# Kernel optimization log

Hardware: AMD Instinct MI355X
Metric: run time of the kernel (lower is better)

## Reference

```python
import jax, jax.numpy as jnp
import numpy as np

P = 2  # sampling ratio: keep top ceil(M/p) measurements


def setup_inputs() -> dict:
    key = jax.random.key(0)
    k1, k2, k3 = jax.random.split(key, 3)
    B, H, W, C = 8, 1024, 1024, 3
    Y = jax.random.normal(k1, (B, H, W, C), dtype=jnp.float32)
    # build()-time Z0 components: abs ~ N(0.5, 0.1), angle ~ N(0, 0.5*sqrt(pi))
    Z0_abs = 0.5 + 0.1 * jax.random.normal(k2, (1, 1, H, W), dtype=jnp.float32)
    Z0_angle = (0.5 * np.pi ** 0.5) * jax.random.normal(k3, (1, 1, H, W), dtype=jnp.float32)
    return {"Y": Y, "Z0_abs": Z0_abs, "Z0_angle": Z0_angle}


def _make_Z0(Z0_abs, Z0_angle):
    # Z0 = |Z0| * exp(i*angle), Frobenius-normalized over spatial axes (2,3)
    Z0 = Z0_abs.astype(jnp.complex64) * jnp.exp(1j * Z0_angle.astype(jnp.complex64))
    fro = jnp.sqrt(jnp.sum(jnp.abs(Z0) ** 2, axis=(2, 3), keepdims=True)).astype(jnp.complex64)
    return Z0 / fro


def reference(Y, Z0_abs, Z0_angle):
    B, H, W, C = Y.shape
    M = H * W * C
    R = int(np.ceil(M / P))
    # transpose NHWC -> NCHW, scale by original S[2] (= W)
    Y_S = jnp.transpose(Y.astype(jnp.float32), (0, 3, 1, 2)) / jnp.float32(W)
    y_s = Y_S.reshape(B, M)
    # threshold = R-th largest value per batch (== descending-sorted index R-1)
    thr = jax.lax.top_k(y_s, R)[0][:, -1]  # [B]
    Ytr = (Y_S >= thr[:, None, None, None]).astype(jnp.float32)  # [B,C,H,W]
    Z0 = _make_Z0(Z0_abs, Z0_angle)
    return Ytr, Z0
```

## Files before the change

kernel.cpp:

```cpp
#include <hip/hip_runtime.h>
#include <math.h>

#define BATCH 8
#define HH 1024
#define WW 1024
#define CC 3
#define MTOT (HH*WW*CC)
#define RSEL 1572864u

#define WCAP 131072u
#define LCAP 1024u
#define P1B  1024
#define QPT  8

#define U_HI 0xBC800000u
#define U_LO 0x437FFFFFu

typedef float nfloat4 __attribute__((ext_vector_type(4)));
typedef float nfloat2 __attribute__((ext_vector_type(2)));

#define WS_WCNT_OFF  0u
#define WS_CHI_OFF   512u
#define WS_NPART_OFF 1024u
#define WS_THR_OFF   2048u
#define WS_FB_OFF    2112u
#define WS_NORM_OFF  2176u
#define WS_WU_OFF    4096u
#define WS_WP_OFF    4198400u

#define NCOPY 3
#define HSTRIDE 4097

__device__ __forceinline__ unsigned int fmap(float x) {
    unsigned int b = __float_as_uint(x);
    return (b & 0x80000000u) ? ~b : (b | 0x80000000u);
}

__device__ __forceinline__ void nt_store4(float4 v, float4* p) {
    nfloat4 t; t.x = v.x; t.y = v.y; t.z = v.z; t.w = v.w;
    __builtin_nontemporal_store(t, (nfloat4*)p);
}
__device__ __forceinline__ void nt_store2(float2 v, float2* p) {
    nfloat2 t; t.x = v.x; t.y = v.y;
    __builtin_nontemporal_store(t, (nfloat2*)p);
}

__device__ __forceinline__ void thresh_row_quad(const float* __restrict__ Yb,
                                                float* __restrict__ outb,
                                                int h, int w4, unsigned int tu) {
    const float4* src = (const float4*)(Yb + ((size_t)h * WW + (size_t)w4 * 4) * CC);
    float4 a0 = src[0], a1 = src[1], a2 = src[2];
    float4 r0, r1, r2;
    r0.x = (fmap(a0.x) >= tu) ? 1.f : 0.f;
    r0.y = (fmap(a0.w) >= tu) ? 1.f : 0.f;
    r0.z = (fmap(a1.z) >= tu) ? 1.f : 0.f;
    r0.w = (fmap(a2.y) >= tu) ? 1.f : 0.f;
    r1.x = (fmap(a0.y) >= tu) ? 1.f : 0.f;
    r1.y = (fmap(a1.x) >= tu) ? 1.f : 0.f;
    r1.z = (fmap(a1.w) >= tu) ? 1.f : 0.f;
    r1.w = (fmap(a2.z) >= tu) ? 1.f : 0.f;
    r2.x = (fmap(a0.z) >= tu) ? 1.f : 0.f;
    r2.y = (fmap(a1.y) >= tu) ? 1.f : 0.f;
    r2.z = (fmap(a2.x) >= tu) ? 1.f : 0.f;
    r2.w = (fmap(a2.w) >= tu) ? 1.f : 0.f;
    size_t base = (size_t)h * WW;
    ((float4*)(outb + base))[w4]                        = r0;
    ((float4*)(outb + base + (size_t)HH * WW))[w4]      = r1;
    ((float4*)(outb + base + (size_t)2 * HH * WW))[w4]  = r2;
}

__global__ void pass1_kernel(const float* __restrict__ Y,
                             const float* __restrict__ zabs,
                             float* __restrict__ out,
                             unsigned int* __restrict__ wu,
                             unsigned int* __restrict__ wpos,
                             unsigned int* __restrict__ wcnt,
                             unsigned int* __restrict__ chib,
                             float* __restrict__ npart) {
    const int tid = threadIdx.x;

    if (blockIdx.x >= P1B) {
        const int bx = blockIdx.x - P1B;
        float s = 0.f;
        const int n4z = HH * WW / 4;
        for (int i = bx * 256 + tid; i < n4z; i += 256 * 256) {
            float4 v = ((const float4*)zabs)[i];
            s += v.x * v.x + v.y * v.y + v.z * v.z + v.w * v.w;
        }
        for (int d = 32; d > 0; d >>= 1) s += __shfl_down(s, d);
        __shared__ float ls[4];
        if ((tid & 63) == 0) ls[tid >> 6] = s;
        __syncthreads();
        if (tid == 0) npart[bx] = ls[0] + ls[1] + ls[2] + ls[3];
        return;
    }

    __shared__ unsigned int lu[LCAP];
    __shared__ unsigned int lp[LCAP];
    __shared__ unsigned int lcnt;
    __shared__ unsigned int red[4];
    __shared__ unsigned int gbase_s;
    if (tid == 0) lcnt = 0u;
    __syncthreads();

    const int blk = blockIdx.x;
    const int b = blk >> 7;
    const int p0 = (blk & 127) * 2048 + tid;
    const float* Yb = Y + (size_t)b * MTOT;
    float* outb = out + (size_t)b * MTOT;
    float4* o4 = (float4*)outb;

    float4 A0[QPT], A1[QPT], A2[QPT];
#pragma unroll
    for (int it = 0; it < QPT; it++) {
        int p = p0 + it * 256;
        const float4* src = (const float4*)(Yb + (size_t)p * 12);
        A0[it] = src[0]; A1[it] = src[1]; A2[it] = src[2];
    }

    unsigned int hcnt = 0u;

#pragma unroll
    for (int it = 0; it < QPT; it++) {
        const int p = p0 + it * 256;
        const unsigned int rowbase = (unsigned int)(4 * p);
        float4 a0 = A0[it], a1 = A1[it], a2 = A2[it];
        float4 r0, r1, r2;

#define SPEC(val, c, k, dst) do { \
        unsigned int u = fmap(val); \
        dst = (u >= U_HI) ? 1.f : 0.f; \
        if (u >= U_HI) hcnt++; \
        else if (u >= U_LO) { \
            unsigned int pp = atomicAdd(&lcnt, 1u); \
            if (pp < LCAP) { lu[pp] = u; lp[pp] = (unsigned int)((c) * HH * WW) + rowbase + (unsigned int)(k); } \
        } \
    } while (0)

        SPEC(a0.x, 0, 0, r0.x); SPEC(a0.w, 0, 1, r0.y); SPEC(a1.z, 0, 2, r0.z); SPEC(a2.y, 0, 3, r0.w);
        SPEC(a0.y, 1, 0, r1.x); SPEC(a1.x, 1, 1, r1.y); SPEC(a1.w, 1, 2, r1.z); SPEC(a2.z, 1, 3, r1.w);
        SPEC(a0.z, 2, 0, r2.x); SPEC(a1.y, 2, 1, r2.y); SPEC(a2.x, 2, 2, r2.z); SPEC(a2.w, 2, 3, r2.w);
#undef SPEC

        nt_store4(r0, &o4[p]);
        nt_store4(r1, &o4[262144 + p]);
        nt_store4(r2, &o4[524288 + p]);
    }

    __syncthreads();
    unsigned int n = lcnt;
    unsigned int nc = (n > LCAP) ? LCAP : n;
    if (tid == 0) {
        unsigned int add = (n > LCAP) ? (WCAP + 1u) : n;
        gbase_s = atomicAdd(&wcnt[b * 16], add);
    }
    for (int d = 32; d > 0; d >>= 1) hcnt += __shfl_down(hcnt, d);
    if ((tid & 63) == 0) red[tid >> 6] = hcnt;
    __syncthreads();
    if (tid == 0) atomicAdd(&chib[b * 16], red[0] + red[1] + red[2] + red[3]);

    unsigned int gbase = gbase_s;
    unsigned int* wub = wu + (size_t)b * WCAP;
    unsigned int* wpb = wpos + (size_t)b * WCAP;
    for (unsigned int j = tid; j < nc; j += 256u) {
        unsigned int q = gbase + j;
        if (q < WCAP) { wub[q] = lu[j]; wpb[q] = lp[j]; }
    }
}

__global__ void __launch_bounds__(1024) refine_kernel(
        const float* __restrict__ Y,
        const unsigned int* __restrict__ wu,
        const unsigned int* __restrict__ wcnt,
        const unsigned int* __restrict__ chib,
        const float* __restrict__ npart,
        unsigned int* __restrict__ thr,
        unsigned int* __restrict__ fbflag,
        float* __restrict__ normsum) {
    const int tid = threadIdx.x;

    if (blockIdx.x == 8) {
        float s = (tid < 256) ? npart[tid] : 0.f;
        for (int d = 32; d > 0; d >>= 1) s += __shfl_down(s, d);
        __shared__ float ls[16];
        if ((tid & 63) == 0) ls[tid >> 6] = s;
        __syncthreads();
        if (tid == 0) {
            float t = 0.f;
            for (int i = 0; i < 16; i++) t += ls[i];
            *normsum = t;
        }
        return;
    }

    __shared__ unsigned int hist[NCOPY * HSTRIDE];
    __shared__ unsigned int waveSums[16];
    __shared__ unsigned int selBin, selBase;
    const int b = blockIdx.x;
    const int lane = tid & 63, wid = tid >> 6;
    const int hc = (wid % NCOPY) * HSTRIDE;

    const unsigned int wc = wcnt[b * 16];
    const unsigned int Ch = chib[b * 16];
    const int fb = (wc > WCAP) || (Ch >= RSEL) || (Ch + wc < RSEL);
    unsigned int target = fb ? RSEL : (RSEL - Ch);
    const unsigned int wcg = (wc > WCAP) ? WCAP : wc;
    const unsigned int* wp = wu + (size_t)b * WCAP;
    const float* Yb = Y + (size_t)b * MTOT;

    unsigned int d1 = 0, d2 = 0;

    for (int level = 0; level < 3; level++) {
        const int nb  = (level < 2) ? 4096 : 256;
        const int bpt = (level < 2) ? 4 : 1;
        for (int i = tid; i < NCOPY * HSTRIDE; i += 1024) hist[i] = 0u;
        if (tid == 0) { selBin = 0u; selBase = 0u; }
        __syncthreads();

#define HISTO(u) do { \
            if (level == 0) atomicAdd(&hist[hc + ((u) >> 20)], 1u); \
            else if (level == 1) { if (((u) >> 20) == d1) atomicAdd(&hist[hc + (((u) >> 8) & 0xFFFu)], 1u); } \
            else { if (((u) >> 8) == ((d1 << 12) | d2)) atomicAdd(&hist[hc + ((u) & 0xFFu)], 1u); } \
        } while (0)

        if (fb) {
            for (unsigned int i = tid; i < (unsigned int)MTOT; i += 1024u) {
                unsigned int u = fmap(Yb[i]);
                HISTO(u);
            }
        } else {
            for (unsigned int i = tid; i < wcg; i += 1024u) {
                unsigned int u = wp[i];
                HISTO(u);
            }
        }
#undef HISTO
        __syncthreads();
        unsigned int c[4] = {0u, 0u, 0u, 0u};
        unsigned int s = 0u;
        const int nthr = nb / bpt;
        if (tid < nthr)
            for (int k = 0; k < bpt; k++) {
                int bin = nb - 1 - (tid * bpt + k);
                c[k] = hist[bin] + hist[HSTRIDE + bin] + hist[2 * HSTRIDE + bin];
                s += c[k];
            }
        unsigned int incl = s;
        for (int d = 1; d < 64; d <<= 1) {
            unsigned int v = __shfl_up(incl, d);
            if (lane >= d) incl += v;
        }
        if (lane == 63) waveSums[wid] = incl;
        __syncthreads();
        if (tid < 16) {
            unsigned int w = waveSums[tid];
            for (int d = 1; d < 16; d <<= 1) {
                unsigned int v = __shfl_up(w, d);
                if (tid >= d) w += v;
            }
            waveSums[tid] = w;
        }
        __syncthreads();
        incl += (wid > 0) ? waveSums[wid - 1] : 0u;
        unsigned int excl = incl - s;
        if (s > 0u && excl < target && incl >= target) {
            unsigned int run = excl;
            for (int k = 0; k < bpt; k++) {
                if (run + c[k] >= target) {
                    selBin = (unsigned int)(nb - 1 - (tid * bpt + k));
                    selBase = run;
                    break;
                }
                run += c[k];
            }
        }
        __syncthreads();
        if (level == 0) d1 = selBin;
        else if (level == 1) d2 = selBin;
        target -= selBase;
        __syncthreads();
    }
    if (tid == 0) {
        thr[b] = (d1 << 20) | (d2 << 8) | selBin;
        fbflag[b] = (unsigned int)fb;
    }
}

__global__ void fixup_z_kernel(const float* __restrict__ Y,
                               const unsigned int* __restrict__ wu,
                               const unsigned int* __restrict__ wpos,
                               const unsigned int* __restrict__ wcnt,
                               const unsigned int* __restrict__ thr,
                               const unsigned int* __restrict__ fbflag,
                               const float* __restrict__ zabs,
                               const float* __restrict__ zang,
                               const float* __restrict__ normsum,
                               float* __restrict__ out,
                               float* __restrict__ outz, int interleaved) {
    const int tid = threadIdx.x;
    if (blockIdx.x < 2048) {
        int i = blockIdx.x * 256 + tid;
        float inv = 1.0f / sqrtf(*normsum);
        float2 a = ((const float2*)zabs)[i];
        float2 g = ((const float2*)zang)[i];
        float s0, c0, s1, c1;
        __sincosf(g.x, &s0, &c0);
        __sincosf(g.y, &s1, &c1);
        if (interleaved) {
            float4 o;
            o.x = a.x * c0 * inv; o.y = a.x * s0 * inv;
            o.z = a.y * c1 * inv; o.w = a.y * s1 * inv;
            nt_store4(o, &((float4*)outz)[i]);
        } else {
            float2 o;
            o.x = a.x * c0 * inv; o.y = a.y * c1 * inv;
            nt_store2(o, &((float2*)outz)[i]);
        }
    } else {
        const int j = blockIdx.x - 2048;
        const int b = j >> 8;
        const unsigned int tu = thr[b];
        float* outb = out + (size_t)b * MTOT;
        if (fbflag[b]) {
            const float* Yb = Y + (size_t)b * MTOT;
            for (int q = (j & 255); q < 1024; q += 256) {
                int pq = q * 256 + tid;
                thresh_row_quad(Yb, outb, pq >> 8, pq & 255, tu);
            }
        } else {
            const unsigned int wc = wcnt[b * 16];
            const unsigned int* wub = wu + (size_t)b * WCAP;
            const unsigned int* wpb = wpos + (size_t)b * WCAP;
            for (unsigned int i = (unsigned int)(j & 255) * 256u + tid; i < wc; i += 65536u) {
                unsigned int u = wub[i];
                unsigned int pos = wpb[i];
                outb[pos] = (u >= tu) ? 1.f : 0.f;
            }
        }
    }
}

extern "C" void kernel_launch(void* const* d_in, const int* in_sizes, int n_in,
                              void* d_out, int out_size, void* d_ws, size_t ws_size,
                              hipStream_t stream) {
    const float* Y    = (const float*)d_in[0];
    const float* zabs = (const float*)d_in[1];
    const float* zang = (const float*)d_in[2];
    float* out = (float*)d_out;

    unsigned char* ws = (unsigned char*)d_ws;
    unsigned int* wcnt  = (unsigned int*)(ws + WS_WCNT_OFF);
    unsigned int* chib  = (unsigned int*)(ws + WS_CHI_OFF);
    float*        npart = (float*)(ws + WS_NPART_OFF);
    unsigned int* thr   = (unsigned int*)(ws + WS_THR_OFF);
    unsigned int* fbf   = (unsigned int*)(ws + WS_FB_OFF);
    float*        norm  = (float*)(ws + WS_NORM_OFF);
    unsigned int* wu    = (unsigned int*)(ws + WS_WU_OFF);
    unsigned int* wpos  = (unsigned int*)(ws + WS_WP_OFF);

    (void)hipMemsetAsync(ws, 0, 1024, stream);

    pass1_kernel<<<P1B + 256, 256, 0, stream>>>(Y, zabs, out, wu, wpos, wcnt, chib, npart);
    refine_kernel<<<9, 1024, 0, stream>>>(Y, wu, wcnt, chib, npart, thr, fbf, norm);

    size_t zoff = (size_t)BATCH * CC * HH * WW;
    int zfloats = out_size - (int)zoff;
    int interleaved = (zfloats >= 2 * HH * WW) ? 1 : 0;
    fixup_z_kernel<<<2048 + 2048, 256, 0, stream>>>(
        Y, wu, wpos, wcnt, thr, fbf, zabs, zang, norm, out, out + zoff, interleaved);
}
```

Baseline: 259.9 us.

## Halve per-thread work in pass1 and batch LDS candidate appends via bitmask

Pass1 now launches twice as many blocks, each thread handling four float4 triples instead of eight, with launch bounds set to four blocks per SM to lift occupancy. The per-element LDS atomic for window candidates is replaced by a 48-bit per-thread mask, followed by one atomicAdd per thread and a serial emit loop. A sched_barrier separates the loads from the compute. This cuts divergent LDS atomics and register pressure, at the cost of more blocks and more global atomics per batch, and it relies on the rest of the launch code matching the new P1B.

```diff
diff --git a/kernel.cpp b/kernel.cpp
--- a/kernel.cpp
+++ b/kernel.cpp
@@ -10,8 +10,8 @@
 
 #define WCAP 131072u
 #define LCAP 1024u
-#define P1B  1024
-#define QPT  8
+#define P1B  2048
+#define QPT  4
 
 #define U_HI 0xBC800000u
 #define U_LO 0x437FFFFFu
@@ -69,7 +69,8 @@
     ((float4*)(outb + base + (size_t)2 * HH * WW))[w4]  = r2;
 }
 
-__global__ void pass1_kernel(const float* __restrict__ Y,
+__global__ void __launch_bounds__(256, 4) pass1_kernel(
+                             const float* __restrict__ Y,
                              const float* __restrict__ zabs,
                              float* __restrict__ out,
                              unsigned int* __restrict__ wu,
@@ -104,8 +105,8 @@
     __syncthreads();
 
     const int blk = blockIdx.x;
-    const int b = blk >> 7;
-    const int p0 = (blk & 127) * 2048 + tid;
+    const int b = blk >> 8;
+    const int p0 = (blk & 255) * 1024 + tid;
     const float* Yb = Y + (size_t)b * MTOT;
     float* outb = out + (size_t)b * MTOT;
     float4* o4 = (float4*)outb;
@@ -117,34 +118,54 @@
         const float4* src = (const float4*)(Yb + (size_t)p * 12);
         A0[it] = src[0]; A1[it] = src[1]; A2[it] = src[2];
     }
+    __builtin_amdgcn_sched_barrier(0);
 
     unsigned int hcnt = 0u;
+    unsigned long long wmask = 0ull;
 
 #pragma unroll
     for (int it = 0; it < QPT; it++) {
         const int p = p0 + it * 256;
-        const unsigned int rowbase = (unsigned int)(4 * p);
         float4 a0 = A0[it], a1 = A1[it], a2 = A2[it];
         float4 r0, r1, r2;
 
-#define SPEC(val, c, k, dst) do { \
+#define CLS(val, dst, j) do { \
         unsigned int u = fmap(val); \
-        dst = (u >= U_HI) ? 1.f : 0.f; \
-        if (u >= U_HI) hcnt++; \
-        else if (u >= U_LO) { \
-            unsigned int pp = atomicAdd(&lcnt, 1u); \
-            if (pp < LCAP) { lu[pp] = u; lp[pp] = (unsigned int)((c) * HH * WW) + rowbase + (unsigned int)(k); } \
-        } \
+        bool hi = (u >= U_HI); \
+        dst = hi ? 1.f : 0.f; \
+        hcnt += hi ? 1u : 0u; \
+        if (!hi && u >= U_LO) wmask |= (1ull << (it * 12 + (j))); \
     } while (0)
 
-        SPEC(a0.x, 0, 0, r0.x); SPEC(a0.w, 0, 1, r0.y); SPEC(a1.z, 0, 2, r0.z); SPEC(a2.y, 0, 3, r0.w);
-        SPEC(a0.y, 1, 0, r1.x); SPEC(a1.x, 1, 1, r1.y); SPEC(a1.w, 1, 2, r1.z); SPEC(a2.z, 1, 3, r1.w);
-        SPEC(a0.z, 2, 0, r2.x); SPEC(a1.y, 2, 1, r2.y); SPEC(a2.x, 2, 2, r2.z); SPEC(a2.w, 2, 3, r2.w);
-#undef SPEC
+        CLS(a0.x, r0.x, 0); CLS(a0.w, r0.y, 1); CLS(a1.z, r0.z, 2); CLS(a2.y, r0.w, 3);
+        CLS(a0.y, r1.x, 4); CLS(a1.x, r1.y, 5); CLS(a1.w, r1.z, 6); CLS(a2.z, r1.w, 7);
+        CLS(a0.z, r2.x, 8); CLS(a1.y, r2.y, 9); CLS(a2.x, r2.z, 10); CLS(a2.w, r2.w, 11);
+#undef CLS
 
         nt_store4(r0, &o4[p]);
         nt_store4(r1, &o4[262144 + p]);
         nt_store4(r2, &o4[524288 + p]);
+    }
+
+    if (wmask) {
+        unsigned int nw = (unsigned int)__popcll(wmask);
+        unsigned int base = atomicAdd(&lcnt, nw);
+#pragma unroll
+        for (int it = 0; it < QPT; it++) {
+            const int p = p0 + it * 256;
+            const unsigned int rb = (unsigned int)(4 * p);
+            float4 a0 = A0[it], a1 = A1[it], a2 = A2[it];
+#define EMIT(val, ch, k, j) do { \
+            if (wmask & (1ull << (it * 12 + (j)))) { \
+                if (base < LCAP) { lu[base] = fmap(val); lp[base] = (unsigned int)((ch) * HH * WW) + rb + (k); } \
+                base++; \
+            } \
+        } while (0)
+            EMIT(a0.x, 0, 0, 0); EMIT(a0.w, 0, 1, 1); EMIT(a1.z, 0, 2, 2); EMIT(a2.y, 0, 3, 3);
+            EMIT(a0.y, 1, 0, 4); EMIT(a1.x, 1, 1, 5); EMIT(a1.w, 1, 2, 6); EMIT(a2.z, 1, 3, 7);
+            EMIT(a0.z, 2, 0, 8); EMIT(a1.y, 2, 1, 9); EMIT(a2.x, 2, 2, 10); EMIT(a2.w, 2, 3, 11);
+#undef EMIT
+        }
     }
 
     __syncthreads();
```

Measured after the change: 256.9 us. Within noise of the previous version (-1.2%).
